# Kernel tuning notes

Measured on AMD Instinct MI355X. Metric: run time of the kernel, lower is better.

The kernel has to match this reference:

```python
import jax, jax.numpy as jnp
import numpy as np

H = 512      # hidden_size
NH = 8       # head_size (num heads)
DH = H // NH # att_size per head
FFN = 2048
B, S = 8, 1024
NEG = -1e9
EPS = 1e-5


def _layernorm(x, g, b):
    mu = jnp.mean(x, axis=-1, keepdims=True)
    var = jnp.var(x, axis=-1, keepdims=True)
    return (x - mu) * jax.lax.rsqrt(var + EPS) * g + b


def setup_inputs() -> dict:
    key = jax.random.key(0)
    ks = jax.random.split(key, 16)
    s = 0.02
    return {
        "x": jax.random.normal(ks[0], (B, S, H), jnp.float32),
        "attn_bias": jax.random.normal(ks[1], (B, S, S), jnp.float32),
        "graph_mask": jax.random.randint(ks[2], (B, S, S), 0, 2, jnp.int32),
        "ln1_g": jnp.ones((H,), jnp.float32),
        "ln1_b": jnp.zeros((H,), jnp.float32),
        "Wq": jax.random.normal(ks[3], (H, H), jnp.float32) * s,
        "bq": jnp.zeros((H,), jnp.float32),
        "Wk": jax.random.normal(ks[4], (H, H), jnp.float32) * s,
        "bk": jnp.zeros((H,), jnp.float32),
        "Wv": jax.random.normal(ks[5], (H, H), jnp.float32) * s,
        "bv": jnp.zeros((H,), jnp.float32),
        "Wo": jax.random.normal(ks[6], (H, H), jnp.float32) * s,
        "bo": jnp.zeros((H,), jnp.float32),
        "ln2_g": jnp.ones((H,), jnp.float32),
        "ln2_b": jnp.zeros((H,), jnp.float32),
        "W1": jax.random.normal(ks[7], (H, FFN), jnp.float32) * s,
        "b1": jnp.zeros((FFN,), jnp.float32),
        "W2": jax.random.normal(ks[8], (FFN, H), jnp.float32) * s,
        "b2": jnp.zeros((H,), jnp.float32),
    }


def reference(x, attn_bias, graph_mask, ln1_g, ln1_b, Wq, bq, Wk, bk, Wv, bv,
              Wo, bo, ln2_g, ln2_b, W1, b1, W2, b2):
    b, s, h = x.shape
    # --- self-attention block (eval mode: dropouts are identity) ---
    y = _layernorm(x, ln1_g, ln1_b)
    q = (y @ Wq + bq).reshape(b, s, NH, DH).transpose(0, 2, 1, 3)  # [B,h,S,d]
    k = (y @ Wk + bk).reshape(b, s, NH, DH).transpose(0, 2, 1, 3)
    v = (y @ Wv + bv).reshape(b, s, NH, DH).transpose(0, 2, 1, 3)
    scale = DH ** -0.5
    scores = jnp.einsum('bhqd,bhkd->bhqk', q * scale, k)  # [B,h,S,S]
    mask = (graph_mask == 0)[:, None, :, :]               # [B,1,S,S] broadcast over heads
    bias = jnp.where(mask, NEG, attn_bias[:, None, :, :])
    scores = scores + bias
    scores = jnp.where(mask, NEG, scores)
    p = jax.nn.softmax(scores, axis=-1)
    o = jnp.einsum('bhqk,bhkd->bhqd', p, v)
    o = o.transpose(0, 2, 1, 3).reshape(b, s, h) @ Wo + bo
    x = x + o
    # --- FFN block ---
    y = _layernorm(x, ln2_g, ln2_b)
    y = jax.nn.gelu(y @ W1 + b1, approximate=False) @ W2 + b2
    return x + y
```

## Files before the change

### kernel.cpp

```cpp
#include <hip/hip_runtime.h>
#include <hip/hip_bf16.h>
#include <type_traits>

static constexpr int kS   = 1024;
static constexpr int kH   = 512;
static constexpr int kFFN = 2048;

using bf16 = __hip_bfloat16;
using short8  = __attribute__((ext_vector_type(8))) short;
using float4v = __attribute__((ext_vector_type(4))) float;
#define MFMA16 __builtin_amdgcn_mfma_f32_16x16x32_bf16

__device__ __forceinline__ unsigned short f2bfu(float f){
  unsigned int u = __float_as_uint(f);
  return (unsigned short)((u + 0x7fffu + ((u >> 16) & 1u)) >> 16);
}
__device__ __forceinline__ float bfu2f(unsigned short u){
  return __uint_as_float(((unsigned int)u) << 16);
}
__device__ __forceinline__ unsigned int pack2(float a, float b){
  return (unsigned int)f2bfu(a) | ((unsigned int)f2bfu(b) << 16);
}
__device__ __forceinline__ void async16(const void* g, void* l){
  __builtin_amdgcn_global_load_lds(
    (const __attribute__((address_space(1))) unsigned int*)g,
    (__attribute__((address_space(3))) unsigned int*)l, 16, 0, 0);
}
__device__ __forceinline__ int swz(int col, int row){
  return (col & ~63) | (((((col>>3)&7) ^ (row&7)))<<3) | (col&7);
}

__device__ __forceinline__ void ln_row(const float* __restrict__ x,
    const float* __restrict__ g, const float* __restrict__ bb,
    bf16* __restrict__ y, long row, int lane){
  const float* xr = x + row * kH + lane*8;
  float4 a = *(const float4*)xr, c = *(const float4*)(xr+4);
  float v[8] = {a.x,a.y,a.z,a.w,c.x,c.y,c.z,c.w};
  float s=0.f, s2=0.f;
#pragma unroll
  for(int i=0;i<8;i++){ s += v[i]; s2 += v[i]*v[i]; }
#pragma unroll
  for(int o=32; o>=1; o>>=1){ s += __shfl_xor(s,o,64); s2 += __shfl_xor(s2,o,64); }
  float mu  = s * (1.f/kH);
  float rs  = rsqrtf(s2*(1.f/kH) - mu*mu + 1e-5f);
  float gv[8], bv[8];
  {
    float4 t0=*(const float4*)(g+lane*8),  t1=*(const float4*)(g+lane*8+4);
    float4 t2=*(const float4*)(bb+lane*8), t3=*(const float4*)(bb+lane*8+4);
    gv[0]=t0.x;gv[1]=t0.y;gv[2]=t0.z;gv[3]=t0.w;gv[4]=t1.x;gv[5]=t1.y;gv[6]=t1.z;gv[7]=t1.w;
    bv[0]=t2.x;bv[1]=t2.y;bv[2]=t2.z;bv[3]=t2.w;bv[4]=t3.x;bv[5]=t3.y;bv[6]=t3.z;bv[7]=t3.w;
  }
  unsigned int ow[4];
#pragma unroll
  for(int i=0;i<4;i++){
    float a0 = (v[2*i]  -mu)*rs*gv[2*i]   + bv[2*i];
    float a1 = (v[2*i+1]-mu)*rs*gv[2*i+1] + bv[2*i+1];
    ow[i] = pack2(a0, a1);
  }
  *reinterpret_cast<uint4*>(y + row*kH + swz(lane*8, (int)row)) = make_uint4(ow[0],ow[1],ow[2],ow[3]);
}

__global__ __launch_bounds__(256) void ln_kernel(const float* __restrict__ x,
    const float* __restrict__ g, const float* __restrict__ bb, bf16* __restrict__ y){
  ln_row(x, g, bb, y, (long)blockIdx.x*4 + (threadIdx.x>>6), threadIdx.x&63);
}

__device__ __forceinline__ void prep_tile(const float* __restrict__ W,
    bf16* __restrict__ WT, int K, int N, int kb, int nb){
  __shared__ unsigned short Ts[64*68];
  int tid=threadIdx.x;
  {
    int k=tid>>2, nc=(tid&3)*16;
    const float* p = W + (size_t)(kb+k)*N + nb+nc;
#pragma unroll
    for(int i=0;i<16;i+=4){
      float4 f = *(const float4*)(p+i);
      Ts[k*68+nc+i  ]=f2bfu(f.x); Ts[k*68+nc+i+1]=f2bfu(f.y);
      Ts[k*68+nc+i+2]=f2bfu(f.z); Ts[k*68+nc+i+3]=f2bfu(f.w);
    }
  }
  __syncthreads();
  {
    int n=tid>>2, kc=(tid&3)*16;
    unsigned short tmp[16];
#pragma unroll
    for(int i=0;i<16;i++) tmp[i] = Ts[(kc+i)*68 + n];
    int row = nb+n, kg0 = kc>>3;
    bf16* op = WT + (size_t)row*K + kb;
    *(uint4*)(op + (((kg0  ^(row&7)))<<3)) = *(uint4*)&tmp[0];
    *(uint4*)(op + ((((kg0+1)^(row&7)))<<3)) = *(uint4*)&tmp[8];
  }
}

__global__ __launch_bounds__(256) void ln1_prep_qkv(
    const float* __restrict__ x, const float* __restrict__ g, const float* __restrict__ bb,
    bf16* __restrict__ y, const float* __restrict__ Wq, const float* __restrict__ Wk,
    const float* __restrict__ Wv, bf16* __restrict__ WT){
  int id = blockIdx.x;
  if(id < 2048){
    ln_row(x, g, bb, y, (long)id*4 + (threadIdx.x>>6), threadIdx.x&63);
  } else {
    int pid = id - 2048, sel = pid>>6, lid = pid&63;
    const float* W = sel==0 ? Wq : (sel==1 ? Wk : Wv);
    prep_tile(W, WT + (size_t)sel*262144, kH, kH, (lid>>3)*64, (lid&7)*64);
  }
}

__global__ __launch_bounds__(256) void prep_rest(
    const float* __restrict__ Wo, const float* __restrict__ W1, const float* __restrict__ W2,
    bf16* __restrict__ WoT, bf16* __restrict__ W1T, bf16* __restrict__ W2T){
  int id = blockIdx.x;
  const float* W; bf16* WT; int K, N, kb, nb;
  if(id < 64)       { W=Wo; WT=WoT; K=kH;   N=kH;   kb=(id>>3)*64;        nb=(id&7)*64; }
  else if(id < 320) { int l=id-64;  W=W1; WT=W1T; K=kH;   N=kFFN; kb=(l>>5)*64; nb=(l&31)*64; }
  else              { int l=id-320; W=W2; WT=W2T; K=kFFN; N=kH;   kb=(l>>3)*64; nb=(l&7)*64; }
  prep_tile(W, WT, K, N, kb, nb);
}

__global__ __launch_bounds__(256) void bias_eff_kernel(
    const int* __restrict__ mask, const float* __restrict__ bias, bf16* __restrict__ be){
  size_t i8 = ((size_t)blockIdx.x*256 + threadIdx.x)*8;
  int4   m0 = *(const int4*)(mask+i8),   m1 = *(const int4*)(mask+i8+4);
  float4 b0 = *(const float4*)(bias+i8), b1 = *(const float4*)(bias+i8+4);
  const unsigned short NEG = f2bfu(-1e9f);
  unsigned short o[8];
  o[0]=m0.x?f2bfu(b0.x):NEG; o[1]=m0.y?f2bfu(b0.y):NEG;
  o[2]=m0.z?f2bfu(b0.z):NEG; o[3]=m0.w?f2bfu(b0.w):NEG;
  o[4]=m1.x?f2bfu(b1.x):NEG; o[5]=m1.y?f2bfu(b1.y):NEG;
  o[6]=m1.z?f2bfu(b1.z):NEG; o[7]=m1.w?f2bfu(b1.w):NEG;
  *(uint4*)((unsigned short*)be + i8) = *(uint4*)o;
}

template<int BM, int BN, typename OutT, bool SCALE, bool GELU, bool RES, bool CSW>
__global__ __launch_bounds__((BM/64)*(BN/64)*64, 3) void mfma_gemm(
    const bf16* __restrict__ A, const bf16* __restrict__ BT,
    const float* __restrict__ bias, const float* __restrict__ res,
    OutT* __restrict__ C, int M, int N, int K)
{
  constexpr int W  = (BM/64)*(BN/64);
  constexpr int NW = BN/64;
  constexpr int AC = (BM/8)/W, BC = (BN/8)/W;
  __shared__ __align__(16) unsigned short As[BM*64];
  __shared__ __align__(16) unsigned short Bs[BN*64];
  int tid=threadIdx.x, lane=tid&63, quad=lane>>4, l16=lane&15;
  int w=__builtin_amdgcn_readfirstlane(tid>>6);
  int wr = w / NW, wc = w % NW;
  int m0=blockIdx.y*BM, n0=blockIdx.x*BN;
  int lr=lane>>3, lc=lane&7;
  float4v acc[4][4] = {};
  for(int k0=0;k0<K;k0+=64){
    __syncthreads();
#pragma unroll
    for(int i=0;i<AC;i++){
      int r = (w*AC+i)*8;
      async16(A + (size_t)(m0+r+lr)*K + k0 + lc*8, &As[r*64]);
    }
#pragma unroll
    for(int i=0;i<BC;i++){
      int r = (w*BC+i)*8;
      async16(BT + (size_t)(n0+r+lr)*K + k0 + lc*8, &Bs[r*64]);
    }
    __syncthreads();
#pragma unroll
    for(int hf=0;hf<2;hf++){
      short8 af[4], bfv[4];
#pragma unroll
      for(int mi=0;mi<4;mi++){
        int row=wr*64+mi*16+l16;
        af[mi]=*(const short8*)&As[row*64 + (((hf*4+quad)^(row&7))<<3)];
      }
#pragma unroll
      for(int ni=0;ni<4;ni++){
        int n=wc*64+ni*16+l16;
        bfv[ni]=*(const short8*)&Bs[n*64 + (((hf*4+quad)^(n&7))<<3)];
      }
#pragma unroll
      for(int ni=0;ni<4;ni++)
#pragma unroll
        for(int mi=0;mi<4;mi++)
          acc[mi][ni]=MFMA16(af[mi],bfv[ni],acc[mi][ni],0,0,0);
    }
  }
#pragma unroll
  for(int ni=0;ni<4;ni++){
    int col=n0+wc*64+ni*16+l16;
    float bc=bias[col];
#pragma unroll
    for(int mi=0;mi<4;mi++){
#pragma unroll
      for(int r=0;r<4;r++){
        int row=m0+wr*64+mi*16+quad*4+r;
        float v=acc[mi][ni][r]+bc;
        if constexpr(SCALE) v*=0.125f;
        if constexpr(GELU)  v=0.5f*v*(1.f+erff(v*0.70710678118f));
        size_t idx=(size_t)row*N+col;
        if constexpr(RES) v+=res[idx];
        if constexpr(std::is_same<OutT,float>::value) C[idx]=v;
        else {
          size_t ix = CSW ? ((size_t)row*N + swz(col,row)) : idx;
          reinterpret_cast<unsigned short*>(C)[ix]=f2bfu(v);
        }
      }
    }
  }
}

__global__ __launch_bounds__(256, 3) void mfma_gemm_qkv(
    const bf16* __restrict__ A, const bf16* __restrict__ BT,
    const float* __restrict__ bq, const float* __restrict__ bk, const float* __restrict__ bv,
    bf16* __restrict__ qo, bf16* __restrict__ ko, bf16* __restrict__ vT, int M, int N, int K)
{
  __shared__ __align__(16) unsigned short As[128*64];
  __shared__ __align__(16) unsigned short Bs[128*64];
  int tid=threadIdx.x, lane=tid&63, quad=lane>>4, l16=lane&15;
  int w=__builtin_amdgcn_readfirstlane(tid>>6);
  int wr = w >> 1, wc = w & 1;
  int m0=blockIdx.y*128, n0=blockIdx.x*128;
  int lr=lane>>3, lc=lane&7;
  float4v acc[4][4] = {};
  for(int k0=0;k0<K;k0+=64){
    __syncthreads();
#pragma unroll
    for(int i=0;i<4;i++){
      int r = (w*4+i)*8;
      async16(A + (size_t)(m0+r+lr)*K + k0 + lc*8, &As[r*64]);
    }
#pragma unroll
    for(int i=0;i<4;i++){
      int r = (w*4+i)*8;
      async16(BT + (size_t)(n0+r+lr)*K + k0 + lc*8, &Bs[r*64]);
    }
    __syncthreads();
#pragma unroll
    for(int hf=0;hf<2;hf++){
      short8 af[4], bfv[4];
#pragma unroll
      for(int mi=0;mi<4;mi++){
        int row=wr*64+mi*16+l16;
        af[mi]=*(const short8*)&As[row*64 + (((hf*4+quad)^(row&7))<<3)];
      }
#pragma unroll
      for(int ni=0;ni<4;ni++){
        int n=wc*64+ni*16+l16;
        bfv[ni]=*(const short8*)&Bs[n*64 + (((hf*4+quad)^(n&7))<<3)];
      }
#pragma unroll
      for(int ni=0;ni<4;ni++)
#pragma unroll
        for(int mi=0;mi<4;mi++)
          acc[mi][ni]=MFMA16(af[mi],bfv[ni],acc[mi][ni],0,0,0);
    }
  }
  int sec = __builtin_amdgcn_readfirstlane(n0 >> 9);
  const float* bp = sec==0 ? bq : (sec==1 ? bk : bv);
  if(sec == 2){
#pragma unroll
    for(int ni=0;ni<4;ni++){
      int cl=(n0+wc*64+ni*16+l16)&511;
      float bc=bp[cl];
#pragma unroll
      for(int mi=0;mi<4;mi++){
        int row0=m0+wr*64+mi*16+quad*4;
        unsigned int p0=pack2(acc[mi][ni][0]+bc, acc[mi][ni][1]+bc);
        unsigned int p1=pack2(acc[mi][ni][2]+bc, acc[mi][ni][3]+bc);
        *reinterpret_cast<uint2*>(reinterpret_cast<unsigned short*>(vT)
            + (size_t)cl*8192 + row0) = make_uint2(p0,p1);
      }
    }
  } else {
    unsigned short* dst = (unsigned short*)(sec==0 ? qo : ko);
    float scl = (sec==0) ? 0.125f : 1.0f;
#pragma unroll
    for(int ni=0;ni<4;ni++){
      int col=n0+wc*64+ni*16+l16, cl=col&511;
      float bc=bp[cl];
#pragma unroll
      for(int mi=0;mi<4;mi++){
#pragma unroll
        for(int r=0;r<4;r++){
          int row=m0+wr*64+mi*16+quad*4+r;
          dst[(size_t)row*512+cl]=f2bfu((acc[mi][ni][r]+bc)*scl);
        }
      }
    }
  }
}

__global__ __launch_bounds__(256,2) void attn_mfma(
    const bf16* __restrict__ q, const bf16* __restrict__ k,
    const bf16* __restrict__ vT, const bf16* __restrict__ be,
    bf16* __restrict__ o)
{
  __shared__ __align__(16) unsigned short Ks[64*64];
  __shared__ __align__(16) unsigned short Vt[64*64];
  __shared__ __align__(16) unsigned short Bt[64*64];
  __shared__ __align__(16) unsigned short Ps[4*16*72];
  int tid=threadIdx.x, lane=tid&63, quad=lane>>4, l16=lane&15;
  int w=__builtin_amdgcn_readfirstlane(tid>>6);
  int q0=blockIdx.x*64, b=blockIdx.y>>3, h=blockIdx.y&7;
  int lr=lane>>3, lc=lane&7;
  const bf16* qp = q + (size_t)(b*kS + q0 + w*16 + l16)*kH + h*64;
  short8 aq0 = *(const short8*)(qp + quad*8);
  short8 aq1 = *(const short8*)(qp + 32 + quad*8);
  float lpart[4]={0.f,0.f,0.f,0.f};
  float4v oacc[4]={};
  int pb = w*16*72;
  int rql = w*16 + quad*4;
  for(int kt=0;kt<16;kt++){
    int kb=kt*64;
    __syncthreads();
#pragma unroll
    for(int i=0;i<2;i++){
      int rr = w*16 + i*8;
      async16(k  + (size_t)(b*kS+kb+rr+lr)*kH + h*64 + ((lc^lr)<<3), &Ks[rr*64]);
      async16(vT + (size_t)(h*64+rr+lr)*8192 + b*kS + kb + ((lc^lr)<<3), &Vt[rr*64]);
      async16(be + (size_t)(b*kS+q0+rr+lr)*kS + kb + ((lc^lr)<<3), &Bt[rr*64]);
    }
    __syncthreads();
    float4v sa[4];
#pragma unroll
    for(int t=0;t<4;t++){
      int krow=t*16+l16, kx=krow&7;
      short8 b0 = *(const short8*)&Ks[krow*64 + ((quad^kx)<<3)];
      short8 b1 = *(const short8*)&Ks[krow*64 + (((4+quad)^kx)<<3)];
      float4v ci;
#pragma unroll
      for(int r=0;r<4;r++){
        int row = rql + r;
        ci[r] = bfu2f(Bt[row*64 + (((t*2+(l16>>3)) ^ (row&7))<<3) + (l16&7)]);
      }
      ci = MFMA16(aq0,b0,ci,0,0,0);
      sa[t]=MFMA16(aq1,b1,ci,0,0,0);
    }
#pragma unroll
    for(int t=0;t<4;t++){
      int kg = t*2 + (l16>>3), j = l16&7;
#pragma unroll
      for(int r=0;r<4;r++){
        float p = __expf(sa[t][r] - 24.f);
        lpart[r] += p;
        int row = quad*4+r;
        Ps[pb + row*72 + ((kg^(row&7))<<3) + j] = f2bfu(p);
      }
    }
    short8 ap0 = *(const short8*)&Ps[pb + l16*72 + ((quad^(l16&7))<<3)];
    short8 ap1 = *(const short8*)&Ps[pb + l16*72 + (((4+quad)^(l16&7))<<3)];
#pragma unroll
    for(int dt=0;dt<4;dt++){
      int vrow=dt*16+l16, vx=vrow&7;
      short8 bv0=*(const short8*)&Vt[vrow*64+((quad^vx)<<3)];
      short8 bv1=*(const short8*)&Vt[vrow*64+(((4+quad)^vx)<<3)];
      oacc[dt]=MFMA16(ap0,bv0,oacc[dt],0,0,0);
      oacc[dt]=MFMA16(ap1,bv1,oacc[dt],0,0,0);
    }
  }
  float inv[4];
#pragma unroll
  for(int r=0;r<4;r++){
    float l = lpart[r];
    l += __shfl_xor(l,1,64); l += __shfl_xor(l,2,64);
    l += __shfl_xor(l,4,64); l += __shfl_xor(l,8,64);
    inv[r] = 1.f/l;
  }
#pragma unroll
  for(int dt=0;dt<4;dt++)
#pragma unroll
    for(int r=0;r<4;r++){
      int row = b*kS + q0 + rql + r;
      int col = h*64 + dt*16 + l16;
      reinterpret_cast<unsigned short*>(o)[(size_t)row*kH + swz(col,row)] =
        f2bfu(oacc[dt][r]*inv[r]);
    }
}

extern "C" void kernel_launch(void* const* d_in, const int* in_sizes, int n_in,
                              void* d_out, int out_size, void* d_ws, size_t ws_size,
                              hipStream_t stream){
  (void)in_sizes; (void)n_in; (void)out_size; (void)ws_size;
  const float* x         = (const float*)d_in[0];
  const float* attn_bias = (const float*)d_in[1];
  const int*   graph_mask= (const int*)  d_in[2];
  const float* ln1_g = (const float*)d_in[3];
  const float* ln1_b = (const float*)d_in[4];
  const float* Wq = (const float*)d_in[5];
  const float* bq = (const float*)d_in[6];
  const float* Wk = (const float*)d_in[7];
  const float* bk = (const float*)d_in[8];
  const float* Wv = (const float*)d_in[9];
  const float* bv = (const float*)d_in[10];
  const float* Wo = (const float*)d_in[11];
  const float* bo = (const float*)d_in[12];
  const float* ln2_g = (const float*)d_in[13];
  const float* ln2_b = (const float*)d_in[14];
  const float* W1 = (const float*)d_in[15];
  const float* b1 = (const float*)d_in[16];
  const float* W2 = (const float*)d_in[17];
  const float* b2 = (const float*)d_in[18];

  char* wsb = (char*)d_ws;
  const size_t SZ = (size_t)8192 * kH * sizeof(bf16);
  bf16* s0 = (bf16*)(wsb);
  bf16* s1 = (bf16*)(wsb + SZ);
  bf16* s2 = (bf16*)(wsb + 2*SZ);
  bf16* s3 = (bf16*)(wsb + 3*SZ);
  float* outf = (float*)d_out;
  bf16*  WqkvT = (bf16*)d_out;
  bf16*  beP   = (bf16*)d_out;
  bf16* WoT = s3;
  bf16* W1T = s3 + 262144;
  bf16* W2T = s3 + 262144 + 1048576;

  dim3 blk(256);
  ln1_prep_qkv<<<dim3(2240), blk, 0, stream>>>(x, ln1_g, ln1_b, s0, Wq, Wk, Wv, WqkvT);
  mfma_gemm_qkv<<<dim3(12,64), blk, 0, stream>>>(s0, WqkvT, bq, bk, bv, s1, s2, s3, 8192, 3*kH, kH);
  bias_eff_kernel<<<dim3(4096), blk, 0, stream>>>(graph_mask, attn_bias, beP);
  attn_mfma<<<dim3(16,64), blk, 0, stream>>>(s1, s2, s3, beP, s0);
  prep_rest<<<dim3(576), blk, 0, stream>>>(Wo, W1, W2, WoT, W1T, W2T);
  mfma_gemm<128,64,float,false,false,true,false><<<dim3(8,64), dim3(128), 0, stream>>>(s0, WoT, bo, x, outf, 8192, kH, kH);
  ln_kernel<<<dim3(2048), blk, 0, stream>>>(outf, ln2_g, ln2_b, s0);
  for(int c=0;c<2;c++){
    size_t ro = (size_t)c * 4096 * kH;
    mfma_gemm<128,128,bf16,false,true ,false,true ><<<dim3(16,32), blk, 0, stream>>>(s0 + ro, W1T, b1, nullptr, s1, 4096, kFFN, kH);
    mfma_gemm<64,64,  float,false,false,true ,false><<<dim3(8,64),  dim3(64), 0, stream>>>(s1, W2T, b2, outf + ro, outf + ro, 4096, kH, kFFN);
  }
}
```

Baseline: 349.1 us.

## Double-buffer attention K/V tiles, load bias directly, add 4-wave 64x64 residual GEMM

The attention kernel now double-buffers the K and V tiles in LDS, prefetching the next tile while computing on the current one. It reads the precomputed bias straight from global memory into registers instead of staging it through LDS, remaps block indices so neighbouring blocks spread across batch/head, and raises the occupancy hint. The Wo and W2 residual GEMMs switch to a new 256-thread kernel with 64x64 tiles and four waves per block, giving more waves in flight. The risks are uncoalesced per-lane bias reads from global memory and extra LDS per attention block from the doubled buffers.

```diff
diff --git a/kernel.cpp b/kernel.cpp
--- a/kernel.cpp
+++ b/kernel.cpp
@@ -205,6 +205,66 @@
   }
 }
 
+__global__ __launch_bounds__(256, 4) void quad_gemm(
+    const bf16* __restrict__ A, const bf16* __restrict__ BT,
+    const float* __restrict__ bias, const float* __restrict__ res,
+    float* __restrict__ C, int M, int N, int K)
+{
+  __shared__ __align__(16) unsigned short As[64*64];
+  __shared__ __align__(16) unsigned short Bs[64*64];
+  int tid=threadIdx.x, lane=tid&63, quad=lane>>4, l16=lane&15;
+  int w=__builtin_amdgcn_readfirstlane(tid>>6);
+  int wr=w>>1, wc=w&1;
+  int m0=blockIdx.y*64, n0=blockIdx.x*64;
+  int lr=lane>>3, lc=lane&7;
+  float4v acc[2][2]={};
+  for(int k0=0;k0<K;k0+=64){
+    __syncthreads();
+#pragma unroll
+    for(int i=0;i<2;i++){
+      int r=(w*2+i)*8;
+      async16(A  + (size_t)(m0+r+lr)*K + k0 + lc*8, &As[r*64]);
+      async16(BT + (size_t)(n0+r+lr)*K + k0 + lc*8, &Bs[r*64]);
+    }
+    __syncthreads();
+#pragma unroll
+    for(int hf=0;hf<2;hf++){
+      short8 af[2], bfv[2];
+#pragma unroll
+      for(int mi=0;mi<2;mi++){
+        int row=wr*32+mi*16+l16;
+        af[mi]=*(const short8*)&As[row*64 + (((hf*4+quad)^(row&7))<<3)];
+      }
+#pragma unroll
+      for(int ni=0;ni<2;ni++){
+        int n=wc*32+ni*16+l16;
+        bfv[ni]=*(const short8*)&Bs[n*64 + (((hf*4+quad)^(n&7))<<3)];
+      }
+#pragma unroll
+      for(int ni=0;ni<2;ni++)
+#pragma unroll
+        for(int mi=0;mi<2;mi++)
+          acc[mi][ni]=MFMA16(af[mi],bfv[ni],acc[mi][ni],0,0,0);
+    }
+  }
+#pragma unroll
+  for(int ni=0;ni<2;ni++){
+    int col=n0+wc*32+ni*16+l16;
+    float bc=bias[col];
+#pragma unroll
+    for(int mi=0;mi<2;mi++){
+#pragma unroll
+      for(int r=0;r<4;r++){
+        int row=m0+wr*32+mi*16+quad*4+r;
+        float v=acc[mi][ni][r]+bc;
+        size_t idx=(size_t)row*N+col;
+        v+=res[idx];
+        C[idx]=v;
+      }
+    }
+  }
+}
+
 __global__ __launch_bounds__(256, 3) void mfma_gemm_qkv(
     const bf16* __restrict__ A, const bf16* __restrict__ BT,
     const float* __restrict__ bq, const float* __restrict__ bk, const float* __restrict__ bv,
@@ -286,18 +346,19 @@
   }
 }
 
-__global__ __launch_bounds__(256,2) void attn_mfma(
+__global__ __launch_bounds__(256,3) void attn_mfma(
     const bf16* __restrict__ q, const bf16* __restrict__ k,
     const bf16* __restrict__ vT, const bf16* __restrict__ be,
     bf16* __restrict__ o)
 {
-  __shared__ __align__(16) unsigned short Ks[64*64];
-  __shared__ __align__(16) unsigned short Vt[64*64];
-  __shared__ __align__(16) unsigned short Bt[64*64];
+  __shared__ __align__(16) unsigned short Ks[2][64*64];
+  __shared__ __align__(16) unsigned short Vt[2][64*64];
   __shared__ __align__(16) unsigned short Ps[4*16*72];
   int tid=threadIdx.x, lane=tid&63, quad=lane>>4, l16=lane&15;
   int w=__builtin_amdgcn_readfirstlane(tid>>6);
-  int q0=blockIdx.x*64, b=blockIdx.y>>3, h=blockIdx.y&7;
+  int lin = blockIdx.y*16 + blockIdx.x;
+  int nid = (lin&7)*128 + (lin>>3);
+  int q0=(nid&15)*64, bh=nid>>4, b=bh>>3, h=bh&7;
   int lr=lane>>3, lc=lane&7;
   const bf16* qp = q + (size_t)(b*kS + q0 + w*16 + l16)*kH + h*64;
   short8 aq0 = *(const short8*)(qp + quad*8);
@@ -306,29 +367,40 @@
   float4v oacc[4]={};
   int pb = w*16*72;
   int rql = w*16 + quad*4;
-  for(int kt=0;kt<16;kt++){
-    int kb=kt*64;
-    __syncthreads();
+  const unsigned short* beRow[4];
+#pragma unroll
+  for(int r=0;r<4;r++)
+    beRow[r] = reinterpret_cast<const unsigned short*>(be) + (size_t)(b*kS+q0+rql+r)*kS + l16;
+
+  auto stage = [&](int kt, int bufi){
+    int kb = kt*64;
 #pragma unroll
     for(int i=0;i<2;i++){
       int rr = w*16 + i*8;
-      async16(k  + (size_t)(b*kS+kb+rr+lr)*kH + h*64 + ((lc^lr)<<3), &Ks[rr*64]);
-      async16(vT + (size_t)(h*64+rr+lr)*8192 + b*kS + kb + ((lc^lr)<<3), &Vt[rr*64]);
-      async16(be + (size_t)(b*kS+q0+rr+lr)*kS + kb + ((lc^lr)<<3), &Bt[rr*64]);
-    }
-    __syncthreads();
+      async16(k  + (size_t)(b*kS+kb+rr+lr)*kH + h*64 + ((lc^lr)<<3), &Ks[bufi][rr*64]);
+      async16(vT + (size_t)(h*64+rr+lr)*8192 + b*kS + kb + ((lc^lr)<<3), &Vt[bufi][rr*64]);
+    }
+  };
+  stage(0,0);
+  __syncthreads();
+  for(int kt=0;kt<16;kt++){
+    int cur=kt&1, kb=kt*64;
+    float bev[4][4];
+#pragma unroll
+    for(int t=0;t<4;t++)
+#pragma unroll
+      for(int r=0;r<4;r++)
+        bev[t][r] = bfu2f(beRow[r][kb + t*16]);
+    if(kt<15) stage(kt+1, cur^1);
     float4v sa[4];
 #pragma unroll
     for(int t=0;t<4;t++){
       int krow=t*16+l16, kx=krow&7;
-      short8 b0 = *(const short8*)&Ks[krow*64 + ((quad^kx)<<3)];
-      short8 b1 = *(const short8*)&Ks[krow*64 + (((4+quad)^kx)<<3)];
+      short8 b0 = *(const short8*)&Ks[cur][krow*64 + ((quad^kx)<<3)];
+      short8 b1 = *(const short8*)&Ks[cur][krow*64 + (((4+quad)^kx)<<3)];
       float4v ci;
 #pragma unroll
-      for(int r=0;r<4;r++){
-        int row = rql + r;
-        ci[r] = bfu2f(Bt[row*64 + (((t*2+(l16>>3)) ^ (row&7))<<3) + (l16&7)]);
-      }
+      for(int r=0;r<4;r++) ci[r] = bev[t][r];
       ci = MFMA16(aq0,b0,ci,0,0,0);
       sa[t]=MFMA16(aq1,b1,ci,0,0,0);
     }
@@ -348,11 +420,12 @@
 #pragma unroll
     for(int dt=0;dt<4;dt++){
       int vrow=dt*16+l16, vx=vrow&7;
-      short8 bv0=*(const short8*)&Vt[vrow*64+((quad^vx)<<3)];
-      short8 bv1=*(const short8*)&Vt[vrow*64+(((4+quad)^vx)<<3)];
+      short8 bv0=*(const short8*)&Vt[cur][vrow*64+((quad^vx)<<3)];
+      short8 bv1=*(const short8*)&Vt[cur][vrow*64+(((4+quad)^vx)<<3)];
       oacc[dt]=MFMA16(ap0,bv0,oacc[dt],0,0,0);
       oacc[dt]=MFMA16(ap1,bv1,oacc[dt],0,0,0);
     }
+    __syncthreads();
   }
   float inv[4];
 #pragma unroll
@@ -416,11 +489,11 @@
   bias_eff_kernel<<<dim3(4096), blk, 0, stream>>>(graph_mask, attn_bias, beP);
   attn_mfma<<<dim3(16,64), blk, 0, stream>>>(s1, s2, s3, beP, s0);
   prep_rest<<<dim3(576), blk, 0, stream>>>(Wo, W1, W2, WoT, W1T, W2T);
-  mfma_gemm<128,64,float,false,false,true,false><<<dim3(8,64), dim3(128), 0, stream>>>(s0, WoT, bo, x, outf, 8192, kH, kH);
+  quad_gemm<<<dim3(8,128), blk, 0, stream>>>(s0, WoT, bo, x, outf, 8192, kH, kH);
   ln_kernel<<<dim3(2048), blk, 0, stream>>>(outf, ln2_g, ln2_b, s0);
   for(int c=0;c<2;c++){
     size_t ro = (size_t)c * 4096 * kH;
     mfma_gemm<128,128,bf16,false,true ,false,true ><<<dim3(16,32), blk, 0, stream>>>(s0 + ro, W1T, b1, nullptr, s1, 4096, kFFN, kH);
-    mfma_gemm<64,64,  float,false,false,true ,false><<<dim3(8,64),  dim3(64), 0, stream>>>(s1, W2T, b2, outf + ro, outf + ro, 4096, kH, kFFN);
-  }
-}
+    quad_gemm<<<dim3(8,64), blk, 0, stream>>>(s1, W2T, b2, outf + ro, outf + ro, 4096, kH, kFFN);
+  }
+}
```

Measured after the change: 330.4 us. 1.06x faster.
